# Performance work log

Hardware: AMD Instinct MI355X
Metric: run time of the kernel (lower is better)

The kernel has to match this reference:

```python
import jax, jax.numpy as jnp
import numpy as np
from jax import lax

B, H, W = 2, 1024, 1024
STRIDE = 32
HF, WF = H // STRIDE, W // STRIDE
C_FM = 2048
A = 9                                       # anchors per location
PRE = 2000                                  # pre-NMS top-k
TOPN = 1000                                 # post-NMS proposals per image
POOL = 7
FC = 256
NUM_CLS = 21
NMS_TH = 0.7


def make_anchors():
    scales = jnp.array([128., 256., 512.])
    ratios = jnp.array([0.5, 1., 2.])
    ws = (scales[:, None] / jnp.sqrt(ratios)[None, :]).reshape(-1)   # [9]
    hs = (scales[:, None] * jnp.sqrt(ratios)[None, :]).reshape(-1)   # [9]
    cx = (jnp.arange(WF) + 0.5) * STRIDE
    cy = (jnp.arange(HF) + 0.5) * STRIDE
    cyg, cxg = jnp.meshgrid(cy, cx, indexing='ij')                   # [HF,WF]
    cxg, cyg = cxg[..., None], cyg[..., None]                        # [HF,WF,1]
    x1 = cxg - ws / 2; y1 = cyg - hs / 2
    x2 = cxg + ws / 2; y2 = cyg + hs / 2
    return jnp.stack([x1, y1, x2, y2], -1).reshape(-1, 4)            # [HF*WF*9,4]


def decode(boxes, deltas):
    w = boxes[..., 2] - boxes[..., 0]
    h = boxes[..., 3] - boxes[..., 1]
    cx = boxes[..., 0] + 0.5 * w
    cy = boxes[..., 1] + 0.5 * h
    dx, dy = deltas[..., 0], deltas[..., 1]
    dw = jnp.clip(deltas[..., 2], -4.0, 4.0)
    dh = jnp.clip(deltas[..., 3], -4.0, 4.0)
    ncx = cx + dx * w; ncy = cy + dy * h
    nw = w * jnp.exp(dw); nh = h * jnp.exp(dh)
    return jnp.stack([ncx - 0.5 * nw, ncy - 0.5 * nh,
                      ncx + 0.5 * nw, ncy + 0.5 * nh], -1)


def clip_boxes(boxes):
    lim = jnp.array([W - 1., H - 1., W - 1., H - 1.])
    return jnp.clip(boxes, 0.0, lim)


def iou_mat(a, b):
    area_a = (a[:, 2] - a[:, 0]) * (a[:, 3] - a[:, 1])
    area_b = (b[:, 2] - b[:, 0]) * (b[:, 3] - b[:, 1])
    lt = jnp.maximum(a[:, None, :2], b[None, :, :2])
    rb = jnp.minimum(a[:, None, 2:], b[None, :, 2:])
    wh = jnp.clip(rb - lt, 0.0)
    inter = wh[..., 0] * wh[..., 1]
    return inter / (area_a[:, None] + area_b[None, :] - inter + 1e-9)


def nms_one(boxes, scores):
    s, idx = lax.top_k(scores, PRE)          # pre-NMS top-k, score-sorted
    b = boxes[idx]                           # [PRE,4]
    iou = iou_mat(b, b)                      # [PRE,PRE]
    ar = jnp.arange(PRE)

    def body(i, keep):
        sup = (iou[i] > NMS_TH) & keep[i] & (ar > i)
        return keep & (~sup)

    keep = lax.fori_loop(0, PRE, body, jnp.ones(PRE, bool))
    ms = jnp.where(keep, s, -1e30)
    s2, j = lax.top_k(ms, TOPN)
    valid = s2 > -1e29
    sel = b[j] * valid[:, None].astype(b.dtype)
    return sel, valid


def roi_align_one(fm, roi):
    # fm: [C,HF,WF], roi: [4] in image coords -> [C,POOL,POOL]
    scale = 1.0 / STRIDE
    x1, y1, x2, y2 = roi[0] * scale, roi[1] * scale, roi[2] * scale, roi[3] * scale
    xs = jnp.clip(x1 + (jnp.arange(POOL) + 0.5) * (x2 - x1) / POOL, 0.0, WF - 1.0)
    ys = jnp.clip(y1 + (jnp.arange(POOL) + 0.5) * (y2 - y1) / POOL, 0.0, HF - 1.0)
    x0 = jnp.floor(xs); y0 = jnp.floor(ys)
    wx = xs - x0; wy = ys - y0
    x0i = x0.astype(jnp.int32); x1i = jnp.minimum(x0i + 1, WF - 1)
    y0i = y0.astype(jnp.int32); y1i = jnp.minimum(y0i + 1, HF - 1)
    gy0 = fm[:, y0i, :]; gy1 = fm[:, y1i, :]          # [C,7,WF]
    f00 = gy0[:, :, x0i]; f01 = gy0[:, :, x1i]        # [C,7,7]
    f10 = gy1[:, :, x0i]; f11 = gy1[:, :, x1i]
    wy_ = wy[None, :, None]; wx_ = wx[None, None, :]
    return (f00 * (1 - wy_) * (1 - wx_) + f01 * (1 - wy_) * wx_
            + f10 * wy_ * (1 - wx_) + f11 * wy_ * wx_)


def conv(x, w, b, stride, padding):
    y = lax.conv_general_dilated(x, w, (stride, stride), padding,
                                 dimension_numbers=('NCHW', 'OIHW', 'NCHW'))
    return y + b[None, :, None, None]


def setup_inputs() -> dict:
    key = jax.random.key(0)
    ks = jax.random.split(key, 12)
    f32 = jnp.float32
    inp = {
        'x': jax.random.normal(ks[0], (B, 3, H, W), f32),
        'backbone_w': jax.random.normal(ks[1], (C_FM, 3, STRIDE, STRIDE), f32) * 0.02,
        'backbone_b': jnp.zeros((C_FM,), f32),
        'rpn_w': jax.random.normal(ks[2], (512, C_FM, 3, 3), f32) * 0.01,
        'rpn_b': jnp.zeros((512,), f32),
        'rpn_cls_w': jax.random.normal(ks[3], (2 * A, 512, 1, 1), f32) * 0.02,
        'rpn_cls_b': jnp.zeros((2 * A,), f32),
        'rpn_reg_w': jax.random.normal(ks[4], (4 * A, 512, 1, 1), f32) * 0.02,
        'rpn_reg_b': jnp.zeros((4 * A,), f32),
        'fc1_w': jax.random.normal(ks[5], (C_FM * POOL * POOL, FC), f32) * 0.005,
        'fc1_b': jnp.zeros((FC,), f32),
        'fc2_w': jax.random.normal(ks[6], (FC, FC), f32) * 0.05,
        'fc2_b': jnp.zeros((FC,), f32),
        'cls_w': jax.random.normal(ks[7], (FC, NUM_CLS), f32) * 0.05,
        'cls_b': jnp.zeros((NUM_CLS,), f32),
        'reg_w': jax.random.normal(ks[8], (FC, 4), f32) * 0.05,
        'reg_b': jnp.zeros((4,), f32),
    }
    return inp


def reference(x, backbone_w, backbone_b, rpn_w, rpn_b, rpn_cls_w, rpn_cls_b,
              rpn_reg_w, rpn_reg_b, fc1_w, fc1_b, fc2_w, fc2_b,
              cls_w, cls_b, reg_w, reg_b):
    # backbone (stride-32 patch conv stand-in for resnet50-small)
    fm = jax.nn.relu(conv(x, backbone_w, backbone_b, STRIDE, 'VALID'))   # [B,2048,32,32]

    anchors = make_anchors()                                             # [N,4], N=HF*WF*9
    anchors = jnp.broadcast_to(anchors, (B,) + anchors.shape)

    # RPN head
    h = jax.nn.relu(conv(fm, rpn_w, rpn_b, 1, 'SAME'))                   # [B,512,32,32]
    cls = conv(h, rpn_cls_w, rpn_cls_b, 1, 'SAME')                       # [B,18,32,32]
    reg = conv(h, rpn_reg_w, rpn_reg_b, 1, 'SAME')                       # [B,36,32,32]
    cls = cls.transpose(0, 2, 3, 1).reshape(B, -1, 2)
    reg = reg.transpose(0, 2, 3, 1).reshape(B, -1, 4)
    fg = jax.nn.softmax(cls, axis=-1)[..., 1]                            # [B,N]

    # proposals: decode -> clip -> NMS filter
    proposals = clip_boxes(decode(anchors, reg))                         # [B,N,4]
    props, valid = jax.vmap(nms_one)(proposals, fg)                      # [B,1000,4], [B,1000]

    # ROI pooling (bilinear, 1 sample/bin, spatial_scale=1/32)
    roi = jax.vmap(jax.vmap(roi_align_one, (None, 0)), (0, 0))(fm, props)  # [B,1000,C,7,7]
    vm = valid.astype(fm.dtype)[..., None]
    roi = roi.reshape(B, TOPN, -1) * vm                                  # [B,1000,100352]

    # detection head
    h1 = jax.nn.relu(jnp.einsum('bnf,fk->bnk', roi, fc1_w) + fc1_b)
    h2 = jax.nn.relu(jnp.einsum('bnk,kj->bnj', h1, fc2_w) + fc2_b)
    cls_scores = (jnp.einsum('bnj,jc->bnc', h2, cls_w) + cls_b) * vm
    reg_preds = (jnp.einsum('bnj,jr->bnr', h2, reg_w) + reg_b) * vm

    detections = clip_boxes(decode(props, reg_preds)) * vm
    return detections, cls_scores
```

## Files before the change

kernel.cpp:

```cpp
#include <hip/hip_runtime.h>

#define PRE 2000
#define TOPN 1000

typedef __attribute__((ext_vector_type(8))) short short8t;
typedef __attribute__((ext_vector_type(4))) float f32x4;
typedef unsigned short ushort_t;

__device__ inline unsigned short bf16_rne(float x) {
    unsigned u = __float_as_uint(x);
    unsigned r = u + 0x7FFFu + ((u >> 16) & 1u);
    return (unsigned short)(r >> 16);
}

__device__ inline void split3_bf16(float x, unsigned short& h, unsigned short& m,
                                   unsigned short& l) {
    h = bf16_rne(x);
    float hf = __uint_as_float((unsigned)h << 16);
    float r1 = x - hf;
    m = bf16_rne(r1);
    float mf = __uint_as_float((unsigned)m << 16);
    l = bf16_rne(r1 - mf);
}


__global__ __launch_bounds__(256, 4) void k_fc1gemm(
    const ushort_t* __restrict__ Aq, const ushort_t* __restrict__ Bq,
    ushort_t* __restrict__ T)
{
    const int flat = blockIdx.x;
    const int xcd  = flat & 7;
    const int jj   = flat >> 3;
    const int wg   = xcd * 196 + jj;
    const int b    = wg / 784;
    const int rem  = wg - b * 784;
    const int nt   = rem >> 3;
    const int mt   = rem & 7;

    const int tid  = threadIdx.x;
    const int wid  = tid >> 6, lane = tid & 63;
    const int wm_g = (wid >> 1) * 4;
    const int wn_g = (wid & 1) * 4;

    f32x4 acc[4][4];
#pragma unroll
    for (int i = 0; i < 4; i++)
#pragma unroll
        for (int j = 0; j < 4; j++) acc[i][j] = (f32x4){0.f, 0.f, 0.f, 0.f};

    const size_t aoff = (size_t)b * 2097152 + (size_t)mt * 262144
                      + (size_t)wm_g * 512 + (size_t)lane * 8;
    const size_t boff = (size_t)nt * 262144 + (size_t)wn_g * 512 + (size_t)lane * 8;
    const ushort_t* pA = Aq + aoff;
    const ushort_t* pB = Bq + boff;

    for (int ks = 0; ks < 64; ks++) {
        const size_t so = (size_t)ks * 4096;
        short8t a[4], bb[4];
#pragma unroll
        for (int f = 0; f < 4; f++) {
            a[f]  = *(const short8t*)(pA + so + f * 512);
            bb[f] = *(const short8t*)(pB + so + f * 512);
        }
#pragma unroll
        for (int mf = 0; mf < 4; mf++)
#pragma unroll
            for (int nf = 0; nf < 4; nf++)
                acc[mf][nf] = __builtin_amdgcn_mfma_f32_16x16x32_bf16(
                    a[mf], bb[nf], acc[mf][nf], 0, 0, 0);
    }

    ushort_t* Tb = T + (size_t)b * 12845056;
    const int rbase = (lane >> 4) * 4;
    const int lrow  = lane & 15;
#pragma unroll
    for (int mf = 0; mf < 4; mf++) {
#pragma unroll
        for (int nf = 0; nf < 4; nf++) {
            int col = nt * 128 + (wn_g + nf) * 16 + lrow;
#pragma unroll
            for (int r = 0; r < 4; r++) {
                int row = mt * 128 + (wm_g + mf) * 16 + rbase + r;
                Tb[(size_t)row * 12544 + col] = bf16_rne(acc[mf][nf][r]);
            }
        }
    }
}


__global__ __launch_bounds__(256, 2) void k_gemm6(
    const ushort_t* __restrict__ A0, const ushort_t* __restrict__ A1,
    const ushort_t* __restrict__ A2,
    const ushort_t* __restrict__ B0, const ushort_t* __restrict__ B1,
    const ushort_t* __restrict__ B2,
    float* __restrict__ C, int ks_per_z, int KS_TOT, int ldc)
{
    const int tid  = threadIdx.x;
    const int wid  = tid >> 6, lane = tid & 63;
    const int wm_g = (wid >> 1) * 4;
    const int wn_g = (wid & 1) * 4;
    const int mt   = blockIdx.x;
    const int nt   = blockIdx.y;
    const int z    = blockIdx.z;

    f32x4 acc[4][4];
#pragma unroll
    for (int i = 0; i < 4; i++)
#pragma unroll
        for (int j = 0; j < 4; j++) acc[i][j] = (f32x4){0.f, 0.f, 0.f, 0.f};

    const size_t aoff = (size_t)mt * KS_TOT * 4096 + (size_t)wm_g * 512 + (size_t)lane * 8;
    const size_t boff = (size_t)nt * KS_TOT * 4096 + (size_t)wn_g * 512 + (size_t)lane * 8;
    const ushort_t* pA0 = A0 + aoff;
    const ushort_t* pA1 = A1 + aoff;
    const ushort_t* pA2 = A2 + aoff;
    const ushort_t* pB0 = B0 + boff;
    const ushort_t* pB1 = B1 + boff;
    const ushort_t* pB2 = B2 + boff;

    const int ks0 = z * ks_per_z;
    for (int ks = ks0; ks < ks0 + ks_per_z; ks++) {
        const size_t so = (size_t)ks * 4096;
        short8t a0[4], a1[4], a2[4], b0[4], b1[4], b2[4];
#pragma unroll
        for (int f = 0; f < 4; f++) {
            a0[f] = *(const short8t*)(pA0 + so + f * 512);
            a1[f] = *(const short8t*)(pA1 + so + f * 512);
            a2[f] = *(const short8t*)(pA2 + so + f * 512);
            b0[f] = *(const short8t*)(pB0 + so + f * 512);
            b1[f] = *(const short8t*)(pB1 + so + f * 512);
            b2[f] = *(const short8t*)(pB2 + so + f * 512);
        }
#pragma unroll
        for (int mf = 0; mf < 4; mf++)
#pragma unroll
            for (int nf = 0; nf < 4; nf++) {
                f32x4 c = acc[mf][nf];
                c = __builtin_amdgcn_mfma_f32_16x16x32_bf16(a0[mf], b0[nf], c, 0, 0, 0);
                c = __builtin_amdgcn_mfma_f32_16x16x32_bf16(a0[mf], b1[nf], c, 0, 0, 0);
                c = __builtin_amdgcn_mfma_f32_16x16x32_bf16(a1[mf], b0[nf], c, 0, 0, 0);
                c = __builtin_amdgcn_mfma_f32_16x16x32_bf16(a0[mf], b2[nf], c, 0, 0, 0);
                c = __builtin_amdgcn_mfma_f32_16x16x32_bf16(a2[mf], b0[nf], c, 0, 0, 0);
                c = __builtin_amdgcn_mfma_f32_16x16x32_bf16(a1[mf], b1[nf], c, 0, 0, 0);
                acc[mf][nf] = c;
            }
    }

    float* Cz = C + (size_t)z * (gridDim.x * 128) * ldc;
    const int rbase = (lane >> 4) * 4;
    const int lrow  = lane & 15;
#pragma unroll
    for (int mf = 0; mf < 4; mf++) {
#pragma unroll
        for (int nf = 0; nf < 4; nf++) {
            int col = nt * 128 + (wn_g + nf) * 16 + lrow;
#pragma unroll
            for (int r = 0; r < 4; r++) {
                int row = mt * 128 + (wm_g + mf) * 16 + rbase + r;
                Cz[(size_t)row * ldc + col] = acc[mf][nf][r];
            }
        }
    }
}


__global__ void k_convW3(const float* __restrict__ src,
                         ushort_t* __restrict__ D0, ushort_t* __restrict__ D1,
                         ushort_t* __restrict__ D2,
                         int K_LD, int k_base, int KS_TOT)
{
    int t = blockIdx.x * 256 + threadIdx.x;
    int per = KS_TOT << 9;
    int mt = t / per, rem = t - mt * per;
    int ks = rem >> 9, g = (rem >> 6) & 7, l = rem & 63;
    int m  = mt * 128 + g * 16 + (l & 15);
    int k0 = k_base + ks * 32 + ((l >> 4) << 3);
    const float* sp = src + (size_t)m * K_LD + k0;
    short8t v0, v1, v2;
#pragma unroll
    for (int j = 0; j < 8; j++) {
        unsigned short h, mm_, lo;
        split3_bf16(sp[j], h, mm_, lo);
        v0[j] = (short)h; v1[j] = (short)mm_; v2[j] = (short)lo;
    }
    *(short8t*)&D0[(size_t)t * 8] = v0;
    *(short8t*)&D1[(size_t)t * 8] = v1;
    *(short8t*)&D2[(size_t)t * 8] = v2;
}

__global__ void k_convX3(const float* __restrict__ X,
                         ushort_t* __restrict__ D0, ushort_t* __restrict__ D1,
                         ushort_t* __restrict__ D2)
{
    int t = blockIdx.x * 256 + threadIdx.x;
    if (t >= 786432) return;
    int per = 96 << 9;
    int nt = t / per, rem = t - nt * per;
    int ks = rem >> 9, g = (rem >> 6) & 7, l = rem & 63;
    int n  = nt * 128 + g * 16 + (l & 15);
    int bimg = n >> 10, pn = n & 1023;
    int oy = pn >> 5, ox = pn & 31;
    int k0 = ks * 32 + ((l >> 4) << 3);
    int ic = k0 >> 10, kr = k0 & 1023;
    int ky = kr >> 5, kx0 = kr & 31;
    const float* sp = X + (((size_t)(bimg * 3 + ic) * 1024) + oy * 32 + ky) * 1024
                        + ox * 32 + kx0;
    short8t v0, v1, v2;
#pragma unroll
    for (int j = 0; j < 8; j++) {
        unsigned short h, mm_, lo;
        split3_bf16(sp[j], h, mm_, lo);
        v0[j] = (short)h; v1[j] = (short)mm_; v2[j] = (short)lo;
    }
    *(short8t*)&D0[(size_t)t * 8] = v0;
    *(short8t*)&D1[(size_t)t * 8] = v1;
    *(short8t*)&D2[(size_t)t * 8] = v2;
}

__global__ void k_convR3(const float* __restrict__ fm,
                         ushort_t* __restrict__ D0, ushort_t* __restrict__ D1,
                         ushort_t* __restrict__ D2, int k_base, int KS_TOT)
{
    int t = blockIdx.x * 256 + threadIdx.x;
    int per = KS_TOT << 9;
    if (t >= 16 * per) return;
    int nt = t / per, rem = t - nt * per;
    int ks = rem >> 9, g = (rem >> 6) & 7, l = rem & 63;
    int n  = nt * 128 + g * 16 + (l & 15);
    int bimg = n >> 10, pn = n & 1023;
    int y = pn >> 5, x = pn & 31;
    int kg = k_base + ks * 32 + ((l >> 4) << 3);
    int ic = kg / 9;
    int r9 = kg - ic * 9;
    int ky = r9 / 3;
    int kx = r9 - ky * 3;
    short8t v0, v1, v2;
#pragma unroll
    for (int j = 0; j < 8; j++) {
        int yy = y + ky - 1, xx = x + kx - 1;
        float v = 0.f;
        if (yy >= 0 && yy < 32 && xx >= 0 && xx < 32)
            v = fm[(((size_t)(bimg * 2048 + ic)) * 32 + yy) * 32 + xx];
        unsigned short h, mm_, lo;
        split3_bf16(v, h, mm_, lo);
        v0[j] = (short)h; v1[j] = (short)mm_; v2[j] = (short)lo;
        kx++;
        if (kx == 3) { kx = 0; ky++; if (ky == 3) { ky = 0; ic++; } }
    }
    *(short8t*)&D0[(size_t)t * 8] = v0;
    *(short8t*)&D1[(size_t)t * 8] = v1;
    *(short8t*)&D2[(size_t)t * 8] = v2;
}


__global__ void k_convA(const float* __restrict__ fm, ushort_t* __restrict__ Aq)
{
    int t = blockIdx.x * 256 + threadIdx.x;
    if (t >= 524288) return;
    int l  = t & 63;
    int g  = (t >> 6) & 7;
    int ks = (t >> 9) & 63;
    int mt = (t >> 15) & 7;
    int b  = t >> 18;
    int p  = mt * 128 + g * 16 + (l & 15);
    int c0 = ks * 32 + (l >> 4) * 8;
    const float* src = fm + ((size_t)(b * 2048 + c0)) * 1024 + p;
    short8t vh;
#pragma unroll
    for (int j = 0; j < 8; j++) vh[j] = (short)bf16_rne(src[(size_t)j * 1024]);
    *(short8t*)&Aq[(size_t)t * 8] = vh;
}

__global__ void k_convB(const float* __restrict__ W1, ushort_t* __restrict__ Bq)
{
    int t = blockIdx.x * 256 + threadIdx.x;
    if (t >= 3211264) return;
    int l  = t & 63;
    int h_ = (t >> 6) & 7;
    int ks = (t >> 9) & 63;
    int nt = t >> 15;
    int n  = nt * 128 + h_ * 16 + (l & 15);
    int c0 = ks * 32 + (l >> 4) * 8;
    const float* src = W1 + (size_t)c0 * 12544 + n;
    short8t vh;
#pragma unroll
    for (int j = 0; j < 8; j++) vh[j] = (short)bf16_rne(src[(size_t)j * 12544]);
    *(short8t*)&Bq[(size_t)t * 8] = vh;
}


__global__ void k_backbone_reduce(const float* __restrict__ Pb, const float* __restrict__ bias,
                                  float* __restrict__ fm)
{
    int idx = blockIdx.x * 256 + threadIdx.x;
    if (idx >= 2048 * 2048) return;
    int oc = idx >> 11, n = idx & 2047;
    float s = Pb[(size_t)oc * 2048 + n]
            + Pb[((size_t)2048 + oc) * 2048 + n]
            + Pb[((size_t)4096 + oc) * 2048 + n];
    s = fmaxf(s + bias[oc], 0.f);
    int b = n >> 10, p = n & 1023;
    fm[((size_t)b * 2048 + oc) * 1024 + p] = s;
}

__global__ void k_rpn_acc(const float* __restrict__ Cp, float* __restrict__ Racc, int first)
{
    int idx = blockIdx.x * 256 + threadIdx.x;
    if (idx >= 512 * 2048) return;
    float s = 0.f;
#pragma unroll
    for (int z = 0; z < 8; z++)
        s += Cp[(size_t)z * 512 * 2048 + idx];
    Racc[idx] = first ? s : (Racc[idx] + s);
}

__global__ void k_rpn_final(const float* __restrict__ Racc, const float* __restrict__ bias,
                            float* __restrict__ hT)
{
    int idx = blockIdx.x * 256 + threadIdx.x;
    if (idx >= 512 * 2048) return;
    int oc = idx >> 11, n = idx & 2047;
    float s = fmaxf(Racc[(size_t)oc * 2048 + n] + bias[oc], 0.f);
    hT[n * 512 + oc] = s;
}


__global__ __launch_bounds__(64) void k_clsreg(
    const float* __restrict__ hT,
    const float* __restrict__ wc, const float* __restrict__ bc_,
    const float* __restrict__ wr, const float* __restrict__ br_,
    float* __restrict__ cls_raw, float* __restrict__ reg_raw)
{
    __shared__ float s[512];
    int n = blockIdx.x, tid = threadIdx.x;
    const float* hp = hT + n * 512;
    *(float4*)&s[tid * 8]     = *(const float4*)&hp[tid * 8];
    *(float4*)&s[tid * 8 + 4] = *(const float4*)&hp[tid * 8 + 4];
    __syncthreads();
    if (tid < 18) {
        float a = bc_[tid];
        const float* w = wc + tid * 512;
        for (int j = 0; j < 512; j++) a = fmaf(s[j], w[j], a);
        cls_raw[n * 18 + tid] = a;
    } else if (tid < 54) {
        int c = tid - 18;
        float a = br_[c];
        const float* w = wr + c * 512;
        for (int j = 0; j < 512; j++) a = fmaf(s[j], w[j], a);
        reg_raw[n * 36 + c] = a;
    }
}

__global__ void k_proposals(const float* __restrict__ cls_raw, const float* __restrict__ reg_raw,
                            float* __restrict__ proposals, float* __restrict__ scores)
{
    int t = blockIdx.x * 256 + threadIdx.x;
    if (t >= 2 * 9216) return;
    int b = t / 9216, n = t - b * 9216;
    int p = n / 9, a = n - p * 9;
    int pi = b * 1024 + p;
    float c0 = cls_raw[pi * 18 + 2 * a], c1 = cls_raw[pi * 18 + 2 * a + 1];
    float m = fmaxf(c0, c1);
    float e0 = expf(c0 - m), e1 = expf(c1 - m);
    float fg = e1 / (e0 + e1);
    float d0 = reg_raw[pi * 36 + 4 * a + 0];
    float d1 = reg_raw[pi * 36 + 4 * a + 1];
    float d2 = reg_raw[pi * 36 + 4 * a + 2];
    float d3 = reg_raw[pi * 36 + 4 * a + 3];
    int y = p >> 5, x = p & 31;
    const float sc[3] = {128.f, 256.f, 512.f};
    const float rt[3] = {0.5f, 1.f, 2.f};
    int si = a / 3, ri = a - si * 3;
    float sq = sqrtf(rt[ri]);
    float aw = sc[si] / sq, ah = sc[si] * sq;
    float cx = (x + 0.5f) * 32.f, cy = (y + 0.5f) * 32.f;
    float x1 = cx - 0.5f * aw, y1 = cy - 0.5f * ah;
    float x2 = cx + 0.5f * aw, y2 = cy + 0.5f * ah;
    float w = x2 - x1, h = y2 - y1;
    float ccx = x1 + 0.5f * w, ccy = y1 + 0.5f * h;
    float dw = fminf(fmaxf(d2, -4.f), 4.f), dh = fminf(fmaxf(d3, -4.f), 4.f);
    float ncx = ccx + d0 * w, ncy = ccy + d1 * h;
    float nw = w * expf(dw), nh = h * expf(dh);
    float px1 = fminf(fmaxf(ncx - 0.5f * nw, 0.f), 1023.f);
    float py1 = fminf(fmaxf(ncy - 0.5f * nh, 0.f), 1023.f);
    float px2 = fminf(fmaxf(ncx + 0.5f * nw, 0.f), 1023.f);
    float py2 = fminf(fmaxf(ncy + 0.5f * nh, 0.f), 1023.f);
    ((float4*)proposals)[t] = make_float4(px1, py1, px2, py2);
    scores[t] = fg;
}

__global__ void k_sort_init(const float* __restrict__ scores, unsigned long long* __restrict__ keys)
{
    int t = blockIdx.x * 256 + threadIdx.x;
    if (t >= 2 * 16384) return;
    int b = t >> 14, i = t & 16383;
    unsigned long long key = 0ull;
    if (i < 9216) {
        unsigned bits = __float_as_uint(scores[b * 9216 + i]);
        key = ((unsigned long long)bits << 32) | (unsigned)(~i);
    }
    keys[t] = key;
}

__global__ __launch_bounds__(512) void k_sort_lds(unsigned long long* __restrict__ keys,
                                                  int kmode, int wcount)
{
    __shared__ unsigned long long s[4096];
    int b = blockIdx.x / wcount, w = blockIdx.x % wcount;
    unsigned long long* g = keys + b * 16384 + w * 4096;
    int tid = threadIdx.x;
#pragma unroll
    for (int t = 0; t < 8; t++) s[tid + t * 512] = g[tid + t * 512];
    __syncthreads();

    if (kmode == 0) {
        for (unsigned k = 2; k <= 4096; k <<= 1) {
            for (unsigned j = k >> 1; j > 0; j >>= 1) {
#pragma unroll
                for (int t = 0; t < 4; t++) {
                    unsigned p = tid + t * 512;
                    unsigned i = ((p & ~(j - 1)) << 1) | (p & (j - 1));
                    unsigned l = i | j;
                    unsigned gi = (w << 12) + i;
                    bool up = ((gi & k) == 0);
                    unsigned long long a = s[i], c = s[l];
                    bool sw = up ? (c > a) : (a > c);
                    if (sw) { s[i] = c; s[l] = a; }
                }
                __syncthreads();
            }
        }
    } else {
        unsigned k = (unsigned)kmode;
        for (unsigned j = 2048; j > 0; j >>= 1) {
#pragma unroll
            for (int t = 0; t < 4; t++) {
                unsigned p = tid + t * 512;
                unsigned i = ((p & ~(j - 1)) << 1) | (p & (j - 1));
                unsigned l = i | j;
                unsigned gi = (w << 12) + i;
                bool up = ((gi & k) == 0);
                unsigned long long a = s[i], c = s[l];
                bool sw = up ? (c > a) : (a > c);
                if (sw) { s[i] = c; s[l] = a; }
            }
            __syncthreads();
        }
    }
#pragma unroll
    for (int t = 0; t < 8; t++) g[tid + t * 512] = s[tid + t * 512];
}

__global__ void k_sort_global(unsigned long long* __restrict__ keys, int kk, int jj)
{
    int t = blockIdx.x * 256 + threadIdx.x;
    if (t >= 2 * 8192) return;
    int b = t >> 13;
    unsigned p = t & 8191;
    unsigned j = (unsigned)jj, k = (unsigned)kk;
    unsigned i = ((p & ~(j - 1)) << 1) | (p & (j - 1));
    unsigned l = i | j;
    bool up = ((i & k) == 0);
    unsigned long long* g = keys + b * 16384;
    unsigned long long a = g[i], c = g[l];
    bool sw = up ? (c > a) : (a > c);
    if (sw) { g[i] = c; g[l] = a; }
}

__global__ void k_gather_top(const unsigned long long* __restrict__ keys,
                             const float* __restrict__ proposals, float* __restrict__ topBoxes)
{
    int t = blockIdx.x * 256 + threadIdx.x;
    if (t >= 2 * PRE) return;
    int b = t / PRE, pos = t - b * PRE;
    unsigned long long key = keys[b * 16384 + pos];
    unsigned idx = ~(unsigned)(key & 0xFFFFFFFFull);
    ((float4*)topBoxes)[t] = ((const float4*)proposals)[b * 9216 + idx];
}

__global__ __launch_bounds__(64) void k_iou(const float* __restrict__ topBoxes,
                                            unsigned* __restrict__ mask)
{
    int blk = blockIdx.x;
    int b = blk / PRE, i = blk - b * PRE;
    int lane = threadIdx.x;
    const float4* boxes = ((const float4*)topBoxes) + b * PRE;
    float4 bi = boxes[i];
    float area_a = (bi.z - bi.x) * (bi.w - bi.y);
    if (lane < 63) {
        unsigned wbits = 0u;
        for (int t = 0; t < 32; t++) {
            int j = lane * 32 + t;
            if (j < PRE && j > i) {
                float4 bj = boxes[j];
                float area_b = (bj.z - bj.x) * (bj.w - bj.y);
                float ltx = fmaxf(bi.x, bj.x), lty = fmaxf(bi.y, bj.y);
                float rbx = fminf(bi.z, bj.z), rby = fminf(bi.w, bj.w);
                float iw = fmaxf(rbx - ltx, 0.f), ih = fmaxf(rby - lty, 0.f);
                float inter = iw * ih;
                float iou = inter / (area_a + area_b - inter + 1e-9f);
                if (iou > 0.7f) wbits |= (1u << t);
            }
        }
        mask[(b * PRE + i) * 63 + lane] = wbits;
    }
}

__global__ __launch_bounds__(64) void k_greedy(const unsigned* __restrict__ mask,
                                               unsigned* __restrict__ keep)
{
    int b = blockIdx.x;
    int lane = threadIdx.x;
    unsigned kw = (lane < 62) ? 0xFFFFFFFFu : (lane == 62 ? 0xFFFFu : 0u);
    const unsigned* mbase = mask + (size_t)b * PRE * 63;
    bool ld = (lane < 63);

    unsigned buf[16];
#pragma unroll
    for (int d = 0; d < 16; d++)
        buf[d] = ld ? mbase[(size_t)d * 63 + lane] : 0u;

    for (int g = 0; g < PRE; g += 16) {
#pragma unroll
        for (int d = 0; d < 16; d++) {
            int i = g + d;
            unsigned row = buf[d];
            int ip = i + 16;
            buf[d] = (ld && ip < PRE) ? mbase[(size_t)ip * 63 + lane] : 0u;
            unsigned wv = (unsigned)__shfl((int)kw, i >> 5);
            if ((wv >> (i & 31)) & 1u)
                kw &= ~row;
        }
    }
    if (lane < 63) keep[b * 63 + lane] = kw;
}

__global__ __launch_bounds__(64) void k_compact(const unsigned* __restrict__ keep,
                                                const float* __restrict__ topBoxes,
                                                float* __restrict__ props, float* __restrict__ validf)
{
    int b = blockIdx.x;
    int lane = threadIdx.x;
    unsigned kw = (lane < 63) ? keep[b * 63 + lane] : 0u;
    int cnt = __popc(kw);
    int inc = cnt;
    for (int off = 1; off < 64; off <<= 1) {
        int v = __shfl_up(inc, off);
        if (lane >= off) inc += v;
    }
    int excl = inc - cnt;
    for (int t = 0; t < 32; t++) {
        if ((kw >> t) & 1u) {
            int rank = excl + __popc(kw & ((1u << t) - 1u));
            if (rank < TOPN) {
                int j = lane * 32 + t;
                ((float4*)props)[b * TOPN + rank] = ((const float4*)topBoxes)[b * PRE + j];
                validf[b * TOPN + rank] = 1.0f;
            }
        }
    }
}

__global__ void k_roico(const float* __restrict__ props, const float* __restrict__ validf,
                        float* __restrict__ roico)
{
    int t = blockIdx.x * 256 + threadIdx.x;
    if (t >= 2 * TOPN) return;
    float* rc = roico + t * 48;
    if (validf[t] == 0.f) {
        for (int u = 0; u < 48; u++) rc[u] = 0.f;
        return;
    }
    float4 box = ((const float4*)props)[t];
    const float scale = 1.f / 32.f;
    float x1 = box.x * scale, y1 = box.y * scale, x2 = box.z * scale, y2 = box.w * scale;
    for (int u = 0; u < 7; u++) {
        float xs = x1 + (u + 0.5f) * (x2 - x1) / 7.f;
        xs = fminf(fmaxf(xs, 0.f), 31.f);
        float x0f = floorf(xs);
        rc[u] = x0f;
        rc[7 + u] = fminf(x0f + 1.f, 31.f);
        rc[14 + u] = xs - x0f;
        float ys = y1 + (u + 0.5f) * (y2 - y1) / 7.f;
        ys = fminf(fmaxf(ys, 0.f), 31.f);
        float y0f = floorf(ys);
        rc[21 + u] = y0f;
        rc[28 + u] = fminf(y0f + 1.f, 31.f);
        rc[35 + u] = ys - y0f;
    }
}

__global__ __launch_bounds__(256) void k_combine(
    const ushort_t* __restrict__ T, const float* __restrict__ roico,
    const float* __restrict__ validf, const float* __restrict__ b1,
    float* __restrict__ h1)
{
    int g = blockIdx.x;
    int b = g / TOPN;
    int tid = threadIdx.x;
    __shared__ float rc[48];
    if (tid < 48) rc[tid] = roico[(size_t)g * 48 + tid];
    __syncthreads();
    float acc = 0.f;
    float vm = validf[g];
    const ushort_t* Tb = T + (size_t)b * 12845056;
    if (vm != 0.f) {
#pragma unroll
        for (int py = 0; py < 7; py++) {
            int y0 = (int)rc[21 + py], y1 = (int)rc[28 + py];
            float wy = rc[35 + py];
#pragma unroll
            for (int px = 0; px < 7; px++) {
                int x0 = (int)rc[px], x1 = (int)rc[7 + px];
                float wx = rc[14 + px];
                int qo = (py * 7 + px) * 256 + tid;
                float f00 = __uint_as_float((unsigned)Tb[(size_t)(y0 * 32 + x0) * 12544 + qo] << 16);
                float f01 = __uint_as_float((unsigned)Tb[(size_t)(y0 * 32 + x1) * 12544 + qo] << 16);
                float f10 = __uint_as_float((unsigned)Tb[(size_t)(y1 * 32 + x0) * 12544 + qo] << 16);
                float f11 = __uint_as_float((unsigned)Tb[(size_t)(y1 * 32 + x1) * 12544 + qo] << 16);
                acc += f00 * (1.f - wy) * (1.f - wx) + f01 * (1.f - wy) * wx
                     + f10 * wy * (1.f - wx) + f11 * wy * wx;
            }
        }
    }
    h1[(size_t)g * 256 + tid] = fmaxf(acc + b1[tid], 0.f);
}

__global__ __launch_bounds__(256) void k_head(
    const float* __restrict__ h1,
    const float* __restrict__ w2, const float* __restrict__ b2,
    const float* __restrict__ wc, const float* __restrict__ bcb,
    const float* __restrict__ wr, const float* __restrict__ brb,
    const float* __restrict__ props, const float* __restrict__ validf,
    float* __restrict__ out)
{
    int g = blockIdx.x;
    int tid = threadIdx.x;
    __shared__ float s1[256], s2v[256], rg[4];
    s1[tid] = h1[(size_t)g * 256 + tid];
    __syncthreads();
    float acc = b2[tid];
    for (int j = 0; j < 256; j++) acc = fmaf(s1[j], w2[j * 256 + tid], acc);
    s2v[tid] = fmaxf(acc, 0.f);
    __syncthreads();
    float vm = validf[g];
    if (tid < 21) {
        float a = bcb[tid];
        for (int j = 0; j < 256; j++) a = fmaf(s2v[j], wc[j * 21 + tid], a);
        out[8000 + g * 21 + tid] = a * vm;
    } else if (tid >= 32 && tid < 36) {
        int r = tid - 32;
        float a = brb[r];
        for (int j = 0; j < 256; j++) a = fmaf(s2v[j], wr[j * 4 + r], a);
        rg[r] = a * vm;
    }
    __syncthreads();
    if (tid == 0) {
        float4 pb = ((const float4*)props)[g];
        float w = pb.z - pb.x, h = pb.w - pb.y;
        float cx = pb.x + 0.5f * w, cy = pb.y + 0.5f * h;
        float dw = fminf(fmaxf(rg[2], -4.f), 4.f), dh = fminf(fmaxf(rg[3], -4.f), 4.f);
        float ncx = cx + rg[0] * w, ncy = cy + rg[1] * h;
        float nw = w * expf(dw), nh = h * expf(dh);
        float x1 = fminf(fmaxf(ncx - 0.5f * nw, 0.f), 1023.f);
        float y1 = fminf(fmaxf(ncy - 0.5f * nh, 0.f), 1023.f);
        float x2 = fminf(fmaxf(ncx + 0.5f * nw, 0.f), 1023.f);
        float y2 = fminf(fmaxf(ncy + 0.5f * nh, 0.f), 1023.f);
        ((float4*)out)[g] = make_float4(x1 * vm, y1 * vm, x2 * vm, y2 * vm);
    }
}


extern "C" void kernel_launch(void* const* d_in, const int* in_sizes, int n_in,
                              void* d_out, int out_size, void* d_ws, size_t ws_size,
                              hipStream_t stream)
{
    const float* x          = (const float*)d_in[0];
    const float* backbone_w = (const float*)d_in[1];
    const float* backbone_b = (const float*)d_in[2];
    const float* rpn_w      = (const float*)d_in[3];
    const float* rpn_b      = (const float*)d_in[4];
    const float* rpn_cls_w  = (const float*)d_in[5];
    const float* rpn_cls_b  = (const float*)d_in[6];
    const float* rpn_reg_w  = (const float*)d_in[7];
    const float* rpn_reg_b  = (const float*)d_in[8];
    const float* fc1_w      = (const float*)d_in[9];
    const float* fc1_b      = (const float*)d_in[10];
    const float* fc2_w      = (const float*)d_in[11];
    const float* fc2_b      = (const float*)d_in[12];
    const float* cls_w      = (const float*)d_in[13];
    const float* cls_b      = (const float*)d_in[14];
    const float* reg_w      = (const float*)d_in[15];
    const float* reg_b      = (const float*)d_in[16];
    float* out = (float*)d_out;

    char* base = (char*)d_ws;
    size_t off = 0;
    auto alloc = [&](size_t bytes) {
        void* p = base + off;
        off = (off + bytes + 255) & ~(size_t)255;
        return p;
    };
    float* fm        = (float*)alloc((size_t)2 * 2048 * 1024 * 4);
    float* Cp        = (float*)alloc((size_t)16 * 512 * 2048 * 4);
    float* hT        = (float*)alloc(2048u * 512 * 4);
    float* Racc      = (float*)alloc(512u * 2048 * 4);
    float* cls_raw   = (float*)alloc(2048u * 18 * 4);
    float* reg_raw   = (float*)alloc(2048u * 36 * 4);
    float* proposals = (float*)alloc(2u * 9216 * 4 * 4);
    float* scores    = (float*)alloc(2u * 9216 * 4);
    unsigned long long* keys = (unsigned long long*)alloc(2u * 16384 * 8);
    float* topBoxes  = (float*)alloc(2u * PRE * 4 * 4);
    unsigned* ioumask= (unsigned*)alloc(2u * PRE * 63 * 4);
    unsigned* keep   = (unsigned*)alloc(2u * 63 * 4);
    float* props     = (float*)alloc(2u * TOPN * 4 * 4);
    float* validf    = (float*)alloc(2u * TOPN * 4);
    float* roico     = (float*)alloc(2u * TOPN * 48 * 4);
    char*  arena     = (char*)alloc(119537664);
    float* h1        = (float*)alloc(2u * TOPN * 256 * 4);

    ushort_t* Wb0 = (ushort_t*)(arena);
    ushort_t* Wb1 = (ushort_t*)(arena + 12582912);
    ushort_t* Wb2 = (ushort_t*)(arena + 25165824);
    ushort_t* Xf0 = (ushort_t*)(arena + 37748736);
    ushort_t* Xf1 = (ushort_t*)(arena + 50331648);
    ushort_t* Xf2 = (ushort_t*)(arena + 62914560);
    ushort_t* Wr0 = (ushort_t*)(arena);
    ushort_t* Wr1 = (ushort_t*)(arena + 4718592);
    ushort_t* Wr2 = (ushort_t*)(arena + 9437184);
    ushort_t* Rb0 = (ushort_t*)(arena + 14155776);
    ushort_t* Rb1 = (ushort_t*)(arena + 33030144);
    ushort_t* Rb2 = (ushort_t*)(arena + 51904512);
    ushort_t* Aq   = (ushort_t*)(arena);
    ushort_t* Tbuf = (ushort_t*)(arena + 16777216);
    ushort_t* Bq   = (ushort_t*)Cp;

    k_convW3<<<3072, 256, 0, stream>>>(backbone_w, Wb0, Wb1, Wb2, 3072, 0, 96);
    k_convX3<<<3072, 256, 0, stream>>>(x, Xf0, Xf1, Xf2);
    k_gemm6<<<dim3(16, 16, 3), 256, 0, stream>>>(Wb0, Wb1, Wb2, Xf0, Xf1, Xf2,
                                                 Cp, 32, 96, 2048);
    k_backbone_reduce<<<(2048 * 2048) / 256, 256, 0, stream>>>(Cp, backbone_b, fm);

    for (int q = 0; q < 4; q++) {
        k_convW3<<<1152, 256, 0, stream>>>(rpn_w, Wr0, Wr1, Wr2, 18432, q * 4608, 144);
        k_convR3<<<4608, 256, 0, stream>>>(fm, Rb0, Rb1, Rb2, q * 4608, 144);
        k_gemm6<<<dim3(4, 16, 8), 256, 0, stream>>>(Wr0, Wr1, Wr2, Rb0, Rb1, Rb2,
                                                    Cp, 18, 144, 2048);
        k_rpn_acc<<<4096, 256, 0, stream>>>(Cp, Racc, q == 0 ? 1 : 0);
    }
    k_rpn_final<<<4096, 256, 0, stream>>>(Racc, rpn_b, hT);

    k_convB<<<12544, 256, 0, stream>>>(fc1_w, Bq);
    k_convA<<<2048, 256, 0, stream>>>(fm, Aq);

    k_clsreg<<<2048, 64, 0, stream>>>(hT, rpn_cls_w, rpn_cls_b, rpn_reg_w, rpn_reg_b,
                                      cls_raw, reg_raw);
    k_proposals<<<(2 * 9216 + 255) / 256, 256, 0, stream>>>(cls_raw, reg_raw, proposals, scores);

    k_sort_init<<<(2 * 16384) / 256, 256, 0, stream>>>(scores, keys);
    k_sort_lds<<<8, 512, 0, stream>>>(keys, 0, 4);
    k_sort_global<<<64, 256, 0, stream>>>(keys, 8192, 4096);
    k_sort_lds<<<8, 512, 0, stream>>>(keys, 8192, 4);
    k_sort_global<<<64, 256, 0, stream>>>(keys, 16384, 8192);
    k_sort_global<<<64, 256, 0, stream>>>(keys, 16384, 4096);
    k_sort_lds<<<2, 512, 0, stream>>>(keys, 16384, 1);
    k_gather_top<<<(2 * PRE + 255) / 256, 256, 0, stream>>>(keys, proposals, topBoxes);

    k_iou<<<2 * PRE, 64, 0, stream>>>(topBoxes, ioumask);
    k_greedy<<<2, 64, 0, stream>>>(ioumask, keep);
    hipMemsetAsync(props, 0, 2u * TOPN * 4 * 4, stream);
    hipMemsetAsync(validf, 0, 2u * TOPN * 4, stream);
    k_compact<<<2, 64, 0, stream>>>(keep, topBoxes, props, validf);
    k_roico<<<(2 * TOPN + 255) / 256, 256, 0, stream>>>(props, validf, roico);

    k_fc1gemm<<<1568, 256, 0, stream>>>(Aq, Bq, Tbuf);
    k_combine<<<2 * TOPN, 256, 0, stream>>>(Tbuf, roico, validf, fc1_b, h1);
    k_head<<<2 * TOPN, 256, 0, stream>>>(h1, fc2_w, fc2_b, cls_w, cls_b, reg_w, reg_b,
                                         props, validf, out);
}
```

Before: 1.008 ms.

## Double-buffer GEMM operand loads and drop per-step shuffles in greedy NMS

The FC GEMM main loop now holds two register sets for A/B fragments and processes two k-steps per iteration. Loads for the next step are issued before the MFMAs on the current step, so global-load latency overlaps with matrix math; the cost is higher register pressure. The greedy NMS loop keeps a private copy of the current keep word, updated from a prefetched diagonal mask word. This takes the cross-lane shuffle out of the serial per-box dependency chain, leaving only one shuffle per 32-box word.

```diff
diff --git a/kernel.cpp b/kernel.cpp
--- a/kernel.cpp
+++ b/kernel.cpp
@@ -54,20 +54,40 @@
     const ushort_t* pA = Aq + aoff;
     const ushort_t* pB = Bq + boff;
 
-    for (int ks = 0; ks < 64; ks++) {
-        const size_t so = (size_t)ks * 4096;
-        short8t a[4], bb[4];
+    short8t aA[4], bA[4], aB[4], bB[4];
+#pragma unroll
+    for (int f = 0; f < 4; f++) {
+        aA[f] = *(const short8t*)(pA + f * 512);
+        bA[f] = *(const short8t*)(pB + f * 512);
+    }
+
+    for (int ks = 0; ks < 64; ks += 2) {
+        const size_t so1 = (size_t)(ks + 1) * 4096;
 #pragma unroll
         for (int f = 0; f < 4; f++) {
-            a[f]  = *(const short8t*)(pA + so + f * 512);
-            bb[f] = *(const short8t*)(pB + so + f * 512);
+            aB[f] = *(const short8t*)(pA + so1 + f * 512);
+            bB[f] = *(const short8t*)(pB + so1 + f * 512);
         }
 #pragma unroll
         for (int mf = 0; mf < 4; mf++)
 #pragma unroll
             for (int nf = 0; nf < 4; nf++)
                 acc[mf][nf] = __builtin_amdgcn_mfma_f32_16x16x32_bf16(
-                    a[mf], bb[nf], acc[mf][nf], 0, 0, 0);
+                    aA[mf], bA[nf], acc[mf][nf], 0, 0, 0);
+        if (ks + 2 < 64) {
+            const size_t so2 = (size_t)(ks + 2) * 4096;
+#pragma unroll
+            for (int f = 0; f < 4; f++) {
+                aA[f] = *(const short8t*)(pA + so2 + f * 512);
+                bA[f] = *(const short8t*)(pB + so2 + f * 512);
+            }
+        }
+#pragma unroll
+        for (int mf = 0; mf < 4; mf++)
+#pragma unroll
+            for (int nf = 0; nf < 4; nf++)
+                acc[mf][nf] = __builtin_amdgcn_mfma_f32_16x16x32_bf16(
+                    aB[mf], bB[nf], acc[mf][nf], 0, 0, 0);
     }
 
     ushort_t* Tb = T + (size_t)b * 12845056;
@@ -516,20 +536,28 @@
     bool ld = (lane < 63);
 
     unsigned buf[16];
-#pragma unroll
-    for (int d = 0; d < 16; d++)
-        buf[d] = ld ? mbase[(size_t)d * 63 + lane] : 0u;
+    unsigned bufg[16];
+#pragma unroll
+    for (int d = 0; d < 16; d++) {
+        buf[d]  = ld ? mbase[(size_t)d * 63 + lane] : 0u;
+        bufg[d] = mbase[(size_t)d * 63 + 0];
+    }
+    unsigned wcur = 0xFFFFFFFFu;
 
     for (int g = 0; g < PRE; g += 16) {
 #pragma unroll
         for (int d = 0; d < 16; d++) {
             int i = g + d;
-            unsigned row = buf[d];
+            if ((i & 31) == 0 && i > 0)
+                wcur = (unsigned)__shfl((int)kw, i >> 5);
+            unsigned row = buf[d], rowg = bufg[d];
             int ip = i + 16;
-            buf[d] = (ld && ip < PRE) ? mbase[(size_t)ip * 63 + lane] : 0u;
-            unsigned wv = (unsigned)__shfl((int)kw, i >> 5);
-            if ((wv >> (i & 31)) & 1u)
+            buf[d]  = (ld && ip < PRE) ? mbase[(size_t)ip * 63 + lane] : 0u;
+            bufg[d] = (ip < PRE) ? mbase[(size_t)ip * 63 + (ip >> 5)] : 0u;
+            if ((wcur >> (i & 31)) & 1u) {
                 kw &= ~row;
+                wcur &= ~rowg;
+            }
         }
     }
     if (lane < 63) keep[b * 63 + lane] = kw;
```

Measured after the change: 1.063 ms. +5.5%, slower.

## Restructure greedy NMS into blocked chunks with parallel tail suppression

Applied to the files above, without the earlier changes.

Rewrites the greedy NMS mask pass from a single 64-lane wave that walks all 2000 rows serially into a 1024-thread block working on 128-row chunks. For each chunk, one thread resolves suppression among the chunk's own words from a shared-memory tile. All 16 waves then OR the masks of kept rows into the remaining keep words in parallel. The aim is to take the serial per-row shuffle and global-load latency chain off the critical path. In exchange the inner resolve is single-threaded, and each chunk adds several block barriers.

```diff
diff --git a/kernel.cpp b/kernel.cpp
--- a/kernel.cpp
+++ b/kernel.cpp
@@ -506,33 +506,92 @@
     }
 }
 
-__global__ __launch_bounds__(64) void k_greedy(const unsigned* __restrict__ mask,
-                                               unsigned* __restrict__ keep)
-{
-    int b = blockIdx.x;
-    int lane = threadIdx.x;
-    unsigned kw = (lane < 62) ? 0xFFFFFFFFu : (lane == 62 ? 0xFFFFu : 0u);
+
+__global__ __launch_bounds__(1024) void k_greedy(const unsigned* __restrict__ mask,
+                                                 unsigned* __restrict__ keep)
+{
+    __shared__ unsigned s_keep[64];
+    __shared__ unsigned s_sub[128][4];
+    __shared__ unsigned s_or[16][64];
+    const int b = blockIdx.x;
+    const int tid = threadIdx.x;
+    const int wv = tid >> 6, lane = tid & 63;
     const unsigned* mbase = mask + (size_t)b * PRE * 63;
-    bool ld = (lane < 63);
-
-    unsigned buf[16];
-#pragma unroll
-    for (int d = 0; d < 16; d++)
-        buf[d] = ld ? mbase[(size_t)d * 63 + lane] : 0u;
-
-    for (int g = 0; g < PRE; g += 16) {
-#pragma unroll
-        for (int d = 0; d < 16; d++) {
-            int i = g + d;
-            unsigned row = buf[d];
-            int ip = i + 16;
-            buf[d] = (ld && ip < PRE) ? mbase[(size_t)ip * 63 + lane] : 0u;
-            unsigned wv = (unsigned)__shfl((int)kw, i >> 5);
-            if ((wv >> (i & 31)) & 1u)
-                kw &= ~row;
-        }
-    }
-    if (lane < 63) keep[b * 63 + lane] = kw;
+
+    if (tid < 63) s_keep[tid] = (tid < 62) ? 0xFFFFFFFFu : 0xFFFFu;
+    __syncthreads();
+
+    for (int c = 0; c < 16; c++) {
+        const int base = c * 128;
+        const int cnt  = (PRE - base < 128) ? (PRE - base) : 128;
+        const int cw   = c * 4;
+
+        if (tid < cnt * 4) {
+            int ii = tid >> 2, wofs = tid & 3;
+            int w = cw + wofs;
+            s_sub[ii][wofs] = (w < 63) ? mbase[(size_t)(base + ii) * 63 + w] : 0u;
+        }
+        __syncthreads();
+
+        if (tid == 0) {
+            unsigned q0 = s_keep[cw];
+            unsigned q1 = (cw + 1 < 63) ? s_keep[cw + 1] : 0u;
+            unsigned q2 = (cw + 2 < 63) ? s_keep[cw + 2] : 0u;
+            unsigned q3 = (cw + 3 < 63) ? s_keep[cw + 3] : 0u;
+            int l0 = cnt < 32 ? cnt : 32;
+            int l1 = cnt < 64 ? cnt : 64;
+            int l2 = cnt < 96 ? cnt : 96;
+            for (int ii = 0; ii < l0; ii++)
+                if ((q0 >> ii) & 1u) {
+                    q0 &= ~s_sub[ii][0]; q1 &= ~s_sub[ii][1];
+                    q2 &= ~s_sub[ii][2]; q3 &= ~s_sub[ii][3];
+                }
+            for (int ii = 32; ii < l1; ii++)
+                if ((q1 >> (ii - 32)) & 1u) {
+                    q0 &= ~s_sub[ii][0]; q1 &= ~s_sub[ii][1];
+                    q2 &= ~s_sub[ii][2]; q3 &= ~s_sub[ii][3];
+                }
+            for (int ii = 64; ii < l2; ii++)
+                if ((q2 >> (ii - 64)) & 1u) {
+                    q0 &= ~s_sub[ii][0]; q1 &= ~s_sub[ii][1];
+                    q2 &= ~s_sub[ii][2]; q3 &= ~s_sub[ii][3];
+                }
+            for (int ii = 96; ii < cnt; ii++)
+                if ((q3 >> (ii - 96)) & 1u) {
+                    q0 &= ~s_sub[ii][0]; q1 &= ~s_sub[ii][1];
+                    q2 &= ~s_sub[ii][2]; q3 &= ~s_sub[ii][3];
+                }
+            s_keep[cw] = q0;
+            if (cw + 1 < 63) s_keep[cw + 1] = q1;
+            if (cw + 2 < 63) s_keep[cw + 2] = q2;
+            if (cw + 3 < 63) s_keep[cw + 3] = q3;
+        }
+        __syncthreads();
+
+        const int tail0 = cw + 4;
+        const int ntail = 63 - tail0;
+        if (ntail > 0) {
+            unsigned acc = 0u;
+            for (int ii = wv; ii < cnt; ii += 16) {
+                unsigned kwrd = s_keep[cw + (ii >> 5)];
+                if ((kwrd >> (ii & 31)) & 1u) {
+                    if (lane < ntail)
+                        acc |= mbase[(size_t)(base + ii) * 63 + tail0 + lane];
+                }
+            }
+            s_or[wv][lane] = acc;
+            __syncthreads();
+            if (tid < ntail) {
+                unsigned o = 0u;
+#pragma unroll
+                for (int v2 = 0; v2 < 16; v2++) o |= s_or[v2][tid];
+                s_keep[tail0 + tid] &= ~o;
+            }
+        }
+        __syncthreads();
+    }
+
+    if (tid < 63) keep[b * 63 + tid] = s_keep[tid];
 }
 
 __global__ __launch_bounds__(64) void k_compact(const unsigned* __restrict__ keep,
@@ -767,7 +826,7 @@
     k_gather_top<<<(2 * PRE + 255) / 256, 256, 0, stream>>>(keys, proposals, topBoxes);
 
     k_iou<<<2 * PRE, 64, 0, stream>>>(topBoxes, ioumask);
-    k_greedy<<<2, 64, 0, stream>>>(ioumask, keep);
+    k_greedy<<<2, 1024, 0, stream>>>(ioumask, keep);
     hipMemsetAsync(props, 0, 2u * TOPN * 4 * 4, stream);
     hipMemsetAsync(validf, 0, 2u * TOPN * 4, stream);
     k_compact<<<2, 64, 0, stream>>>(keep, topBoxes, props, validf);
```

After: 1.011 ms. No clear change (+0.4%).

## Fuse IoU mask and greedy NMS into one block-wise LDS kernel

Applied to the files above, without the earlier changes.

Replaces the full pairwise IoU bitmask kernel and the serial greedy scan with one kernel per image that processes boxes in chunks of 64. Each chunk resolves its own suppression within a wavefront using ballots, then the whole block suppresses later boxes only against the chunk's survivors. Boxes already suppressed are skipped. This removes the global IoU mask write and read and much of the redundant IoU work. In exchange only 2 blocks run, with 32 serialized chunk steps and barriers between them.

```diff
diff --git a/kernel.cpp b/kernel.cpp
--- a/kernel.cpp
+++ b/kernel.cpp
@@ -478,61 +478,88 @@
     ((float4*)topBoxes)[t] = ((const float4*)proposals)[b * 9216 + idx];
 }
 
-__global__ __launch_bounds__(64) void k_iou(const float* __restrict__ topBoxes,
-                                            unsigned* __restrict__ mask)
-{
-    int blk = blockIdx.x;
-    int b = blk / PRE, i = blk - b * PRE;
-    int lane = threadIdx.x;
-    const float4* boxes = ((const float4*)topBoxes) + b * PRE;
-    float4 bi = boxes[i];
-    float area_a = (bi.z - bi.x) * (bi.w - bi.y);
-    if (lane < 63) {
-        unsigned wbits = 0u;
-        for (int t = 0; t < 32; t++) {
-            int j = lane * 32 + t;
-            if (j < PRE && j > i) {
-                float4 bj = boxes[j];
-                float area_b = (bj.z - bj.x) * (bj.w - bj.y);
-                float ltx = fmaxf(bi.x, bj.x), lty = fmaxf(bi.y, bj.y);
-                float rbx = fminf(bi.z, bj.z), rby = fminf(bi.w, bj.w);
-                float iw = fmaxf(rbx - ltx, 0.f), ih = fmaxf(rby - lty, 0.f);
-                float inter = iw * ih;
-                float iou = inter / (area_a + area_b - inter + 1e-9f);
-                if (iou > 0.7f) wbits |= (1u << t);
-            }
-        }
-        mask[(b * PRE + i) * 63 + lane] = wbits;
-    }
-}
-
-__global__ __launch_bounds__(64) void k_greedy(const unsigned* __restrict__ mask,
-                                               unsigned* __restrict__ keep)
-{
-    int b = blockIdx.x;
-    int lane = threadIdx.x;
-    unsigned kw = (lane < 62) ? 0xFFFFFFFFu : (lane == 62 ? 0xFFFFu : 0u);
-    const unsigned* mbase = mask + (size_t)b * PRE * 63;
-    bool ld = (lane < 63);
-
-    unsigned buf[16];
-#pragma unroll
-    for (int d = 0; d < 16; d++)
-        buf[d] = ld ? mbase[(size_t)d * 63 + lane] : 0u;
-
-    for (int g = 0; g < PRE; g += 16) {
-#pragma unroll
-        for (int d = 0; d < 16; d++) {
-            int i = g + d;
-            unsigned row = buf[d];
-            int ip = i + 16;
-            buf[d] = (ld && ip < PRE) ? mbase[(size_t)ip * 63 + lane] : 0u;
-            unsigned wv = (unsigned)__shfl((int)kw, i >> 5);
-            if ((wv >> (i & 31)) & 1u)
-                kw &= ~row;
-        }
-    }
-    if (lane < 63) keep[b * 63 + lane] = kw;
+
+__global__ __launch_bounds__(1024) void k_nms(const float* __restrict__ topBoxes,
+                                              unsigned* __restrict__ keep)
+{
+    __shared__ float4 bx[PRE];
+    __shared__ unsigned s_keep[64];
+    __shared__ unsigned char s_klist[64];
+    __shared__ int s_kcnt;
+    const int b = blockIdx.x;
+    const int tid = threadIdx.x;
+    const int wv = tid >> 6, lane = tid & 63;
+
+    for (int i = tid; i < PRE; i += 1024)
+        bx[i] = ((const float4*)topBoxes)[b * PRE + i];
+    if (tid < 64) s_keep[tid] = (tid < 62) ? 0xFFFFFFFFu : (tid == 62 ? 0xFFFFu : 0u);
+    __syncthreads();
+
+    for (int c = 0; c < 32; c++) {
+        const int base = c * 64;
+        const int cnt = (PRE - base < 64) ? (PRE - base) : 64;
+
+        if (wv == 0) {
+            unsigned long long col = 0ull;
+            if (lane < cnt) {
+                float4 bl = bx[base + lane];
+                float area_l = (bl.z - bl.x) * (bl.w - bl.y);
+                for (int i = 0; i < lane; i++) {
+                    float4 bi = bx[base + i];
+                    float area_i = (bi.z - bi.x) * (bi.w - bi.y);
+                    float ltx = fmaxf(bi.x, bl.x), lty = fmaxf(bi.y, bl.y);
+                    float rbx = fminf(bi.z, bl.z), rby = fminf(bi.w, bl.w);
+                    float iw = fmaxf(rbx - ltx, 0.f), ih = fmaxf(rby - lty, 0.f);
+                    float inter = iw * ih;
+                    float iou = inter / (area_i + area_l - inter + 1e-9f);
+                    if (iou > 0.7f) col |= (1ull << i);
+                }
+            }
+            unsigned long long alive = ((unsigned long long)s_keep[2 * c + 1] << 32)
+                                     | (unsigned long long)s_keep[2 * c];
+            for (int i = 0; i < cnt; i++) {
+                if ((alive >> i) & 1ull) {
+                    unsigned long long sup = __ballot((unsigned)((col >> i) & 1ull));
+                    alive &= ~sup;
+                }
+            }
+            if (lane < cnt && ((alive >> lane) & 1ull)) {
+                int rank = __popcll(alive & ((1ull << lane) - 1ull));
+                s_klist[rank] = (unsigned char)lane;
+            }
+            if (lane == 0) {
+                s_kcnt = (int)__popcll(alive);
+                s_keep[2 * c] = (unsigned)alive;
+                if (2 * c + 1 < 63) s_keep[2 * c + 1] = (unsigned)(alive >> 32);
+            }
+        }
+        __syncthreads();
+
+        const int kcnt = s_kcnt;
+        if (kcnt > 0) {
+            for (int j = base + 64 + tid; j < PRE; j += 1024) {
+                unsigned w = s_keep[j >> 5];
+                if (!((w >> (j & 31)) & 1u)) continue;
+                float4 bj = bx[j];
+                float area_j = (bj.z - bj.x) * (bj.w - bj.y);
+                bool dead = false;
+                for (int t = 0; t < kcnt; t++) {
+                    float4 bi = bx[base + s_klist[t]];
+                    float area_i = (bi.z - bi.x) * (bi.w - bi.y);
+                    float ltx = fmaxf(bi.x, bj.x), lty = fmaxf(bi.y, bj.y);
+                    float rbx = fminf(bi.z, bj.z), rby = fminf(bi.w, bj.w);
+                    float iw = fmaxf(rbx - ltx, 0.f), ih = fmaxf(rby - lty, 0.f);
+                    float inter = iw * ih;
+                    float iou = inter / (area_i + area_j - inter + 1e-9f);
+                    if (iou > 0.7f) { dead = true; break; }
+                }
+                if (dead) atomicAnd(&s_keep[j >> 5], ~(1u << (j & 31)));
+            }
+        }
+        __syncthreads();
+    }
+
+    if (tid < 63) keep[b * 63 + tid] = s_keep[tid];
 }
 
 __global__ __launch_bounds__(64) void k_compact(const unsigned* __restrict__ keep,
@@ -711,7 +738,6 @@
     float* scores    = (float*)alloc(2u * 9216 * 4);
     unsigned long long* keys = (unsigned long long*)alloc(2u * 16384 * 8);
     float* topBoxes  = (float*)alloc(2u * PRE * 4 * 4);
-    unsigned* ioumask= (unsigned*)alloc(2u * PRE * 63 * 4);
     unsigned* keep   = (unsigned*)alloc(2u * 63 * 4);
     float* props     = (float*)alloc(2u * TOPN * 4 * 4);
     float* validf    = (float*)alloc(2u * TOPN * 4);
@@ -766,8 +792,7 @@
     k_sort_lds<<<2, 512, 0, stream>>>(keys, 16384, 1);
     k_gather_top<<<(2 * PRE + 255) / 256, 256, 0, stream>>>(keys, proposals, topBoxes);
 
-    k_iou<<<2 * PRE, 64, 0, stream>>>(topBoxes, ioumask);
-    k_greedy<<<2, 64, 0, stream>>>(ioumask, keep);
+    k_nms<<<2, 1024, 0, stream>>>(topBoxes, keep);
     hipMemsetAsync(props, 0, 2u * TOPN * 4 * 4, stream);
     hipMemsetAsync(validf, 0, 2u * TOPN * 4, stream);
     k_compact<<<2, 64, 0, stream>>>(keep, topBoxes, props, validf);
```

New measurement: 1.519 ms. 1.51x slower.
